# Kernel optimization log

Measured on AMD Instinct MI355X. Metric: run time of the kernel, lower is better.

Reference implementation:

```python
import jax, jax.numpy as jnp
import numpy as np

B, L1, L2 = 128, 256, 256
EMBED, HIDDEN, OUT = 512, 1024, 3


def _mlp(x, w1, b1, w2, b2):
    # MLPLayer (dropout is identity in eval): ReLU(ReLU(x W1^T + b1) W2^T + b2)
    h = jax.nn.relu(x @ w1.T + b1)
    return jax.nn.relu(h @ w2.T + b2)


def setup_inputs() -> dict:
    key = jax.random.key(0)
    ks = jax.random.split(key, 18)
    s = 0.05
    inp = {
        'sent1': jax.random.normal(ks[0], (B, L1, EMBED), jnp.float32),
        'sent2': jax.random.normal(ks[1], (B, L2, EMBED), jnp.float32),
        # attend MLP f: embed -> hidden -> hidden
        'f_w1': jax.random.normal(ks[2], (HIDDEN, EMBED), jnp.float32) * s,
        'f_b1': jnp.zeros((HIDDEN,), jnp.float32),
        'f_w2': jax.random.normal(ks[3], (HIDDEN, HIDDEN), jnp.float32) * s,
        'f_b2': jnp.zeros((HIDDEN,), jnp.float32),
        # compare MLP g: 2*embed -> hidden -> hidden
        'g_w1': jax.random.normal(ks[4], (HIDDEN, 2 * EMBED), jnp.float32) * s,
        'g_b1': jnp.zeros((HIDDEN,), jnp.float32),
        'g_w2': jax.random.normal(ks[5], (HIDDEN, HIDDEN), jnp.float32) * s,
        'g_b2': jnp.zeros((HIDDEN,), jnp.float32),
        # aggregate MLP h: 2*hidden -> hidden -> hidden
        'h_w1': jax.random.normal(ks[6], (HIDDEN, 2 * HIDDEN), jnp.float32) * s,
        'h_b1': jnp.zeros((HIDDEN,), jnp.float32),
        'h_w2': jax.random.normal(ks[7], (HIDDEN, HIDDEN), jnp.float32) * s,
        'h_b2': jnp.zeros((HIDDEN,), jnp.float32),
        # final linear: hidden -> out
        'fin_w': jax.random.normal(ks[8], (OUT, HIDDEN), jnp.float32) * s,
        'fin_b': jnp.zeros((OUT,), jnp.float32),
    }
    return inp


def reference(sent1, sent2, f_w1, f_b1, f_w2, f_b2, g_w1, g_b1, g_w2, g_b2,
              h_w1, h_b1, h_w2, h_b2, fin_w, fin_b):
    # ---- Attend ----
    f1 = _mlp(sent1, f_w1, f_b1, f_w2, f_b2)            # [B, L1, H]
    f2 = _mlp(sent2, f_w1, f_b1, f_w2, f_b2)            # [B, L2, H]
    e1 = jnp.einsum('bih,bjh->bij', f1, f2)             # [B, L1, L2], no scaling
    w1a = jax.nn.softmax(e1, axis=-1)                    # softmax over L2
    w2a = jax.nn.softmax(jnp.swapaxes(e1, 1, 2), axis=-1)  # [B, L2, L1], softmax over L1
    att1 = jnp.einsum('bij,bje->bie', w1a, sent2)       # [B, L1, E]
    att2 = jnp.einsum('bji,bie->bje', w2a, sent1)       # [B, L2, E]
    # ---- Compare ----
    cmp1 = _mlp(jnp.concatenate([att1, sent1], axis=2), g_w1, g_b1, g_w2, g_b2)  # [B, L1, H]
    cmp2 = _mlp(jnp.concatenate([att2, sent2], axis=2), g_w1, g_b1, g_w2, g_b2)  # [B, L2, H]
    # ---- Aggregate ----
    s1 = jnp.sum(cmp1, axis=1)                          # [B, H]
    s2 = jnp.sum(cmp2, axis=1)                          # [B, H]
    h = _mlp(jnp.concatenate([s1, s2], axis=1), h_w1, h_b1, h_w2, h_b2)
    return h @ fin_w.T + fin_b                          # [B, OUT]
```

## Files before the change

### kernel.cpp

```cpp
#include <hip/hip_runtime.h>
#include <hip/hip_bf16.h>


using f32x4 = __attribute__((ext_vector_type(4))) float;
using s16x8 = __attribute__((ext_vector_type(8))) short;

__device__ __forceinline__ void gload_lds16(const short* g, short* l) {
  __builtin_amdgcn_global_load_lds(
      (const __attribute__((address_space(1))) unsigned int*)g,
      (__attribute__((address_space(3))) unsigned int*)l, 16, 0, 0);
}

template <bool RELU, bool OUT_BF16, bool HAS_BIAS, bool SUML, bool CONCAT>
__global__ __launch_bounds__(256, 4) void gemm_nt(
    const short* __restrict__ A, const short* __restrict__ B,
    const float* __restrict__ bias, void* __restrict__ Cv, int K, int lda,
    int ldb, int ldc, long sA, long sB, long sC, const float* __restrict__ cs1,
    const float* __restrict__ cs2, int cBh) {
  __shared__ __align__(16) short As[128 * 64];
  __shared__ __align__(16) short Bs[128 * 64];
  const int t = threadIdx.x;
  const int lane = t & 63;
  const int wave = t >> 6;

  unsigned flat = (blockIdx.z * gridDim.y + blockIdx.y) * gridDim.x + blockIdx.x;
  const unsigned total = gridDim.x * gridDim.y * gridDim.z;
  unsigned bx = blockIdx.x, by = blockIdx.y, bz = blockIdx.z;
  if ((total & 7u) == 0) {
    unsigned nf = (flat & 7u) * (total >> 3) + (flat >> 3);
    bx = nf % gridDim.x;
    unsigned rest = nf / gridDim.x;
    by = rest % gridDim.y;
    bz = rest / gridDim.y;
  }
  const int m0 = by * 128;
  const int n0 = bx * 128;
  const long zb = bz;

  const int srow = t >> 3;
  const int schunk = ((t & 7) ^ (srow & 7)) * 8;
  const short* ag = A + zb * sA + (long)(m0 + srow) * lda + schunk;
  const short* bg = B + zb * sB + (long)(n0 + srow) * ldb + schunk;
  const long a32 = (long)32 * lda, b32 = (long)32 * ldb;
  short* AsW = As + wave * 512;
  short* BsW = Bs + wave * 512;

  const int fr = lane & 15;
  const int kq = lane >> 4;
  int aoff[4], boff[4];
#pragma unroll
  for (int i = 0; i < 4; ++i) {
    const int ra = (wave >> 1) * 64 + i * 16 + fr;
    const int rb = (wave & 1) * 64 + i * 16 + fr;
    aoff[i] = ra * 64 + ((kq ^ (ra & 7)) * 8);
    boff[i] = rb * 64 + ((kq ^ (rb & 7)) * 8);
  }

  f32x4 acc[4][4] = {};

  for (int it = K >> 6; it > 0; --it) {
    gload_lds16(ag, AsW);
    gload_lds16(ag + a32, AsW + 2048);
    gload_lds16(ag + 2 * a32, AsW + 4096);
    gload_lds16(ag + 3 * a32, AsW + 6144);
    gload_lds16(bg, BsW);
    gload_lds16(bg + b32, BsW + 2048);
    gload_lds16(bg + 2 * b32, BsW + 4096);
    gload_lds16(bg + 3 * b32, BsW + 6144);
    ag += 64;
    bg += 64;
    __syncthreads();
#pragma unroll
    for (int kk = 0; kk < 2; ++kk) {
      const int x = kk * 32;
      s16x8 af[4], bfv[4];
#pragma unroll
      for (int i = 0; i < 4; ++i) af[i] = *(const s16x8*)(As + (aoff[i] ^ x));
#pragma unroll
      for (int j = 0; j < 4; ++j) bfv[j] = *(const s16x8*)(Bs + (boff[j] ^ x));
#pragma unroll
      for (int i = 0; i < 4; ++i)
#pragma unroll
        for (int j = 0; j < 4; ++j)
          acc[i][j] = __builtin_amdgcn_mfma_f32_16x16x32_bf16(
              af[i], bfv[j], acc[i][j], 0, 0, 0);
    }
    __syncthreads();
  }

  const int ccol = lane & 15;
  const int crow = (lane >> 4) * 4;

  if constexpr (SUML) {
    __shared__ float ssum[128];
    if (t < 128) ssum[t] = 0.f;
    __syncthreads();
#pragma unroll
    for (int j = 0; j < 4; ++j) {
      const int lcol = (wave & 1) * 64 + j * 16 + ccol;
      float bj = HAS_BIAS ? bias[n0 + lcol] : 0.f;
      float part = 0.f;
#pragma unroll
      for (int i = 0; i < 4; ++i)
#pragma unroll
        for (int r = 0; r < 4; ++r) {
          float x = acc[i][j][r] + bj;
          if (RELU) x = fmaxf(x, 0.f);
          part += x;
        }
      atomicAdd(&ssum[lcol], part);
    }
    __syncthreads();
    if (t < 128) {
      const int split = (int)sC;
      int rb2 = m0 >> 8;
      const int side = rb2 >= split;
      rb2 -= side * split;
      atomicAdd((float*)Cv + (long)rb2 * ldc + side * (ldc >> 1) + n0 + t,
                ssum[t]);
    }
  } else {
#pragma unroll
    for (int j = 0; j < 4; ++j) {
      const int col = n0 + (wave & 1) * 64 + j * 16 + ccol;
      float bj = 0.f;
      if (HAS_BIAS) bj = bias[col];
#pragma unroll
      for (int i = 0; i < 4; ++i) {
        const int row0 = m0 + (wave >> 1) * 64 + i * 16 + crow;
#pragma unroll
        for (int r = 0; r < 4; ++r) {
          float x = acc[i][j][r] + bj;
          if (RELU) x = fmaxf(x, 0.f);
          const long idx = (long)(row0 + r) * ldc + col + zb * sC;
          if (OUT_BF16)
            ((__hip_bfloat16*)Cv)[idx] = __float2bfloat16(x);
          else
            ((float*)Cv)[idx] = x;
        }
      }
    }
    if constexpr (CONCAT) {
      const int side = (int)(zb >= (long)cBh);
      const int bb = (int)zb - side * cBh;
      const float* csrc = side ? cs2 : cs1;
      const long crowbase = (long)bb * 256;
      __hip_bfloat16* Cb = (__hip_bfloat16*)Cv + zb * sC + 512 + n0;
#pragma unroll
      for (int k = 0; k < 16; ++k) {
        const int idx = k * 256 + t;
        const int r = idx >> 5;
        const int q = idx & 31;
        const float4 v =
            *(const float4*)(csrc + (crowbase + m0 + r) * 512 + n0 + q * 4);
        union {
          ushort4 u;
          __hip_bfloat16 h[4];
        } pk;
        pk.h[0] = __float2bfloat16(v.x);
        pk.h[1] = __float2bfloat16(v.y);
        pk.h[2] = __float2bfloat16(v.z);
        pk.h[3] = __float2bfloat16(v.w);
        *(ushort4*)(Cb + (long)(m0 + r) * ldc + q * 4) = pk.u;
      }
    }
  }
}

struct CastArgs {
  const float* src[6];
  __hip_bfloat16* dst[6];
  long n[6];
};
__global__ void cast_many(CastArgs a) {
  const int w = blockIdx.y;
  long i = ((long)blockIdx.x * blockDim.x + threadIdx.x) * 4;
  if (i >= a.n[w]) return;
  float4 v = *(const float4*)(a.src[w] + i);
  __hip_bfloat16* o = a.dst[w] + i;
  o[0] = __float2bfloat16(v.x);
  o[1] = __float2bfloat16(v.y);
  o[2] = __float2bfloat16(v.z);
  o[3] = __float2bfloat16(v.w);
}

__global__ void cast_bf16(const float* __restrict__ in,
                          __hip_bfloat16* __restrict__ out, long n) {
  long i = ((long)blockIdx.x * blockDim.x + threadIdx.x) * 4;
  if (i >= n) return;
  float4 v = *(const float4*)(in + i);
  out[i + 0] = __float2bfloat16(v.x);
  out[i + 1] = __float2bfloat16(v.y);
  out[i + 2] = __float2bfloat16(v.z);
  out[i + 3] = __float2bfloat16(v.w);
}

__global__ void prep_sent(const float* __restrict__ s1,
                          const float* __restrict__ s2,
                          __hip_bfloat16* __restrict__ S12b,
                          __hip_bfloat16* __restrict__ STbase, int Bh) {
  __shared__ float tile[32][33];
  const int z = blockIdx.z;
  const int e0 = blockIdx.x * 32;
  const int l0 = blockIdx.y * 32;
  const int side = z >= Bh;
  const int b = z - side * Bh;
  const float* ib = (side ? s2 : s1) + (long)b * 131072;
  __hip_bfloat16* on = S12b + (long)z * 131072;
  __hip_bfloat16* ot = STbase + (long)(side ? b : (Bh + b)) * 131072;
  const int tx = threadIdx.x, ty = threadIdx.y;
#pragma unroll
  for (int k = 0; k < 4; ++k) {
    const int l = l0 + ty + 8 * k;
    const float v = ib[(long)l * 512 + e0 + tx];
    on[(long)l * 512 + e0 + tx] = __float2bfloat16(v);
    tile[ty + 8 * k][tx] = v;
  }
  __syncthreads();
#pragma unroll
  for (int k = 0; k < 4; ++k)
    ot[(long)(e0 + ty + 8 * k) * 256 + l0 + tx] =
        __float2bfloat16(tile[tx][ty + 8 * k]);
}

__global__ void softmax_rows(const float* __restrict__ E,
                             __hip_bfloat16* __restrict__ W) {
  const long row = blockIdx.x;
  const int t = threadIdx.x;
  const float x = E[row * 256 + t];
  float m = x;
  for (int o = 32; o > 0; o >>= 1) m = fmaxf(m, __shfl_xor(m, o));
  __shared__ float red[4];
  if ((t & 63) == 0) red[t >> 6] = m;
  __syncthreads();
  m = fmaxf(fmaxf(red[0], red[1]), fmaxf(red[2], red[3]));
  const float pr = __expf(x - m);
  float s = pr;
  for (int o = 32; o > 0; o >>= 1) s += __shfl_xor(s, o);
  __shared__ float red2[4];
  if ((t & 63) == 0) red2[t >> 6] = s;
  __syncthreads();
  s = red2[0] + red2[1] + red2[2] + red2[3];
  W[row * 256 + t] = __float2bfloat16(pr / s);
}

__global__ __launch_bounds__(256) void softmax_cols_f(
    const float* __restrict__ E, __hip_bfloat16* __restrict__ W) {
  __shared__ float tile[256][65];
  __shared__ float mred[4][64], sred[4][64];
  const int b = blockIdx.y;
  const int j0 = blockIdx.x * 64;
  const int t = threadIdx.x;
  const int jl = t & 63, s = t >> 6;
  const float* Eb = E + (long)b * 65536 + j0;
#pragma unroll
  for (int k = 0; k < 64; ++k) {
    const int i = k * 4 + s;
    tile[i][jl] = Eb[(long)i * 256 + jl];
  }
  __syncthreads();
  float m = -3.4e38f;
#pragma unroll 8
  for (int r = 0; r < 64; ++r) m = fmaxf(m, tile[s * 64 + r][jl]);
  mred[s][jl] = m;
  __syncthreads();
  m = fmaxf(fmaxf(mred[0][jl], mred[1][jl]), fmaxf(mred[2][jl], mred[3][jl]));
  float sum = 0.f;
#pragma unroll 8
  for (int r = 0; r < 64; ++r) sum += __expf(tile[s * 64 + r][jl] - m);
  sred[s][jl] = sum;
  __syncthreads();
  const int jw = t >> 2;
  const int ib = t & 3;
  const float mj = fmaxf(fmaxf(mred[0][jw], mred[1][jw]),
                         fmaxf(mred[2][jw], mred[3][jw]));
  const float isj =
      1.0f / (sred[0][jw] + sred[1][jw] + sred[2][jw] + sred[3][jw]);
  __hip_bfloat16* Wb = W + (long)b * 65536 + (long)(j0 + jw) * 256 + ib * 64;
#pragma unroll 8
  for (int r = 0; r < 64; ++r)
    Wb[r] = __float2bfloat16(__expf(tile[ib * 64 + r][jw] - mj) * isj);
}

__global__ void final_lin(const __hip_bfloat16* __restrict__ h2,
                          const float* __restrict__ w,
                          const float* __restrict__ bs,
                          float* __restrict__ out) {
  const int b = blockIdx.x;
  const int t = threadIdx.x;
  float p0 = 0.f, p1 = 0.f, p2 = 0.f;
  for (int k = t; k < 1024; k += 256) {
    const float x = __bfloat162float(h2[(long)b * 1024 + k]);
    p0 += x * w[k];
    p1 += x * w[1024 + k];
    p2 += x * w[2048 + k];
  }
  for (int o = 32; o > 0; o >>= 1) {
    p0 += __shfl_xor(p0, o);
    p1 += __shfl_xor(p1, o);
    p2 += __shfl_xor(p2, o);
  }
  __shared__ float r[4][3];
  if ((t & 63) == 0) {
    r[t >> 6][0] = p0;
    r[t >> 6][1] = p1;
    r[t >> 6][2] = p2;
  }
  __syncthreads();
  if (t < 3)
    out[b * 3 + t] = r[0][t] + r[1][t] + r[2][t] + r[3][t] + bs[t];
}

extern "C" void kernel_launch(void* const* d_in, const int* in_sizes, int n_in,
                              void* d_out, int out_size, void* d_ws,
                              size_t ws_size, hipStream_t stream) {
  const float* sent1 = (const float*)d_in[0];
  const float* sent2 = (const float*)d_in[1];
  const float* f_w1 = (const float*)d_in[2];
  const float* f_b1 = (const float*)d_in[3];
  const float* f_w2 = (const float*)d_in[4];
  const float* f_b2 = (const float*)d_in[5];
  const float* g_w1 = (const float*)d_in[6];
  const float* g_b1 = (const float*)d_in[7];
  const float* g_w2 = (const float*)d_in[8];
  const float* g_b2 = (const float*)d_in[9];
  const float* h_w1 = (const float*)d_in[10];
  const float* h_b1 = (const float*)d_in[11];
  const float* h_w2 = (const float*)d_in[12];
  const float* h_b2 = (const float*)d_in[13];
  const float* fin_w = (const float*)d_in[14];
  const float* fin_b = (const float*)d_in[15];

  char* p = (char*)d_ws;
  auto take = [&](size_t n) {
    char* r = p;
    p += (n + 255) & ~(size_t)255;
    return r;
  };
  const int Bh = (ws_size >= (size_t)220 * 1024 * 1024) ? 64 : 32;
  const int chunks = 128 / Bh;
  const long R = (long)Bh * 256;

  short* Wf1 = (short*)take(1024L * 512 * 2);
  short* Wf2 = (short*)take(1024L * 1024 * 2);
  short* Wg1 = (short*)take(1024L * 1024 * 2);
  short* Wg2 = (short*)take(1024L * 1024 * 2);
  short* Wh1 = (short*)take(1024L * 2048 * 2);
  short* Wh2 = (short*)take(1024L * 1024 * 2);
  float* SUMF = (float*)take(128L * 2048 * 4);
  short* scat = (short*)take(128L * 2048 * 2);
  short* hh = (short*)take(128L * 1024 * 2);
  short* hf = (short*)take(128L * 1024 * 2);
  char* Areg = take(2 * R * 1024 * 2);
  char* Breg = take(2 * R * 1024 * 2);
  char* Creg = take(2 * R * 512 * 2);
  char* Dreg = take(2 * R * 512 * 2);
  (void)in_sizes; (void)n_in; (void)out_size;

  short* FHID = (short*)Areg;
  short* GHID = (short*)Areg;
  short* F12 = (short*)Breg;
  short* CC12 = (short*)Breg;
  short* S12b = (short*)Creg;
  float* E1 = (float*)Creg;
  short* W1A = (short*)(Creg + (long)Bh * 262144);
  short* W2A = W1A + (long)Bh * 65536;
  short* ST = (short*)Dreg;

  hipMemsetAsync(SUMF, 0, 128L * 2048 * 4, stream);

  CastArgs ca;
  ca.src[0] = f_w1; ca.dst[0] = (__hip_bfloat16*)Wf1; ca.n[0] = 524288;
  ca.src[1] = f_w2; ca.dst[1] = (__hip_bfloat16*)Wf2; ca.n[1] = 1048576;
  ca.src[2] = g_w1; ca.dst[2] = (__hip_bfloat16*)Wg1; ca.n[2] = 1048576;
  ca.src[3] = g_w2; ca.dst[3] = (__hip_bfloat16*)Wg2; ca.n[3] = 1048576;
  ca.src[4] = h_w1; ca.dst[4] = (__hip_bfloat16*)Wh1; ca.n[4] = 2097152;
  ca.src[5] = h_w2; ca.dst[5] = (__hip_bfloat16*)Wh2; ca.n[5] = 1048576;
  cast_many<<<dim3(2048, 6), 256, 0, stream>>>(ca);

  for (int c = 0; c < chunks; ++c) {
    const float* s1 = sent1 + (long)c * R * 512;
    const float* s2 = sent2 + (long)c * R * 512;
    float* SUMF_c = SUMF + (long)c * Bh * 2048;
    const int MT = (int)(2 * R / 128);

    prep_sent<<<dim3(16, 8, 2 * Bh), dim3(32, 8), 0, stream>>>(
        s1, s2, (__hip_bfloat16*)S12b, (__hip_bfloat16*)ST, Bh);

    gemm_nt<true, true, true, false, false><<<dim3(8, MT, 1), 256, 0, stream>>>(
        S12b, Wf1, f_b1, FHID, 512, 512, 512, 1024, 0, 0, 0, nullptr, nullptr, 0);
    gemm_nt<true, true, true, false, false><<<dim3(8, MT, 1), 256, 0, stream>>>(
        FHID, Wf2, f_b2, F12, 1024, 1024, 1024, 1024, 0, 0, 0, nullptr, nullptr, 0);

    gemm_nt<false, false, false, false, false><<<dim3(2, 2, Bh), 256, 0, stream>>>(
        F12, F12 + R * 1024, nullptr, E1, 1024, 1024, 1024, 256, 256L * 1024,
        256L * 1024, 65536, nullptr, nullptr, 0);

    softmax_rows<<<Bh * 256, 256, 0, stream>>>(E1, (__hip_bfloat16*)W1A);
    softmax_cols_f<<<dim3(4, Bh), 256, 0, stream>>>(E1, (__hip_bfloat16*)W2A);

    gemm_nt<false, true, false, false, true><<<dim3(4, 2, 2 * Bh), 256, 0, stream>>>(
        W1A, ST, nullptr, CC12, 256, 256, 256, 1024, 65536, 131072, 262144,
        s1, s2, Bh);

    gemm_nt<true, true, true, false, false><<<dim3(8, MT, 1), 256, 0, stream>>>(
        CC12, Wg1, g_b1, GHID, 1024, 1024, 1024, 1024, 0, 0, 0, nullptr, nullptr, 0);
    gemm_nt<true, false, true, true, false><<<dim3(8, MT, 1), 256, 0, stream>>>(
        GHID, Wg2, g_b2, SUMF_c, 1024, 1024, 1024, 2048, 0, 0, Bh, nullptr, nullptr, 0);
  }

  cast_bf16<<<256, 256, 0, stream>>>(SUMF, (__hip_bfloat16*)scat, 262144);
  gemm_nt<true, true, true, false, false><<<dim3(8, 1, 1), 256, 0, stream>>>(
      scat, Wh1, h_b1, hh, 2048, 2048, 2048, 1024, 0, 0, 0, nullptr, nullptr, 0);
  gemm_nt<true, true, true, false, false><<<dim3(8, 1, 1), 256, 0, stream>>>(
      hh, Wh2, h_b2, hf, 1024, 1024, 1024, 1024, 0, 0, 0, nullptr, nullptr, 0);
  final_lin<<<128, 256, 0, stream>>>((__hip_bfloat16*)hf, fin_w, fin_b,
                                     (float*)d_out);
}
```

Measured before the change: 901.5 us.

## Add 256x256-tile 8-wave pipelined GEMM for the four big MLP layers

Adds a new GEMM kernel with 256x256 output tiles, 512 threads and a four-stage LDS pipeline built on direct global-to-LDS loads. Reads from LDS and MFMA work are interleaved through explicit barriers, waitcnt instructions and priority hints, with XOR swizzling to avoid bank conflicts. The kernel replaces the 128-tile kernel for the f and g MLP GEMMs, and its sum variant first reduces over rows in LDS before issuing global atomics. Larger tiles raise arithmetic intensity and reuse, at the cost of fewer blocks, lower occupancy and more register pressure.

```diff
diff --git a/kernel.cpp b/kernel.cpp
--- a/kernel.cpp
+++ b/kernel.cpp
@@ -9,6 +9,223 @@
   __builtin_amdgcn_global_load_lds(
       (const __attribute__((address_space(1))) unsigned int*)g,
       (__attribute__((address_space(3))) unsigned int*)l, 16, 0, 0);
+}
+
+template <bool SUML>
+__global__ __launch_bounds__(512, 2) void gemm256(
+    const short* __restrict__ A, const short* __restrict__ B,
+    const float* __restrict__ bias, void* __restrict__ Cv, int K, int lda,
+    int ldb, int ldc, int split) {
+  __shared__ __align__(16) short As[2 * 2 * 8192];
+  __shared__ __align__(16) short Bs[2 * 2 * 8192];
+
+  const int t = threadIdx.x;
+  const int lane = t & 63;
+  const int w = t >> 6;
+  const int wm = w >> 2;
+  const int wn = w & 3;
+
+  unsigned bx = blockIdx.x, by = blockIdx.y;
+  {
+    unsigned flat = by * gridDim.x + bx;
+    unsigned total = gridDim.x * gridDim.y;
+    if ((total & 7u) == 0) {
+      unsigned nf = (flat & 7u) * (total >> 3) + (flat >> 3);
+      bx = nf % gridDim.x;
+      by = nf / gridDim.x;
+    }
+  }
+  const int m0 = by * 256;
+  const int n0 = bx * 256;
+
+  const short* gA[2];
+  const short* gB[2];
+  short* lA[2];
+  short* lB[2];
+#pragma unroll
+  for (int q = 0; q < 2; ++q) {
+    const int r = (w * 2 + q) * 16 + (lane >> 2);
+    const int cg = (lane & 3) ^ ((r >> 1) & 3);
+    gA[q] = A + (long)(m0 + r) * lda + cg * 8;
+    gB[q] = B + (long)(n0 + r) * ldb + cg * 8;
+    lA[q] = As + (w * 2 + q) * 512;
+    lB[q] = Bs + (w * 2 + q) * 512;
+  }
+
+  const int c4 = lane >> 4;
+  const int rA0 = wm * 128 + (lane & 15);
+  const int rB0 = wn * 64 + (lane & 15);
+  const int aoff0 = rA0 * 32 + ((c4 ^ ((rA0 >> 1) & 3)) * 8);
+  const int boff0 = rB0 * 32 + ((c4 ^ ((rB0 >> 1) & 3)) * 8);
+
+  f32x4 acc[8][4] = {};
+  s16x8 af[8], bf[2];
+
+  const int nIter = K >> 7;
+
+  auto stgA = [&](int koff, int roff) {
+#pragma unroll
+    for (int q = 0; q < 2; ++q) gload_lds16(gA[q] + koff, lA[q] + roff);
+  };
+  auto stgB = [&](int koff, int roff) {
+#pragma unroll
+    for (int q = 0; q < 2; ++q) gload_lds16(gB[q] + koff, lB[q] + roff);
+  };
+  auto rdA = [&](int reg) {
+#pragma unroll
+    for (int m = 0; m < 8; ++m)
+      af[m] = *(const s16x8*)(As + reg + aoff0 + m * 512);
+  };
+  auto rdB = [&](int reg, int np) {
+#pragma unroll
+    for (int n = 0; n < 2; ++n)
+      bf[n] = *(const s16x8*)(Bs + reg + boff0 + (np * 2 + n) * 512);
+  };
+  auto mf16 = [&](int np) {
+    __builtin_amdgcn_s_setprio(1);
+#pragma unroll
+    for (int m = 0; m < 8; ++m)
+#pragma unroll
+      for (int n = 0; n < 2; ++n)
+        acc[m][np * 2 + n] = __builtin_amdgcn_mfma_f32_16x16x32_bf16(
+            af[m], bf[n], acc[m][np * 2 + n], 0, 0, 0);
+    __builtin_amdgcn_s_setprio(0);
+  };
+
+  stgA(0, 0);
+  stgB(0, 0);
+  stgA(32, 8192);
+  stgB(32, 8192);
+  stgA(64, 16384);
+  stgB(64, 16384);
+  asm volatile("s_waitcnt vmcnt(4)" ::: "memory");
+  __builtin_amdgcn_sched_barrier(0);
+  __builtin_amdgcn_s_barrier();
+
+  for (int i = 0; i < nIter; ++i) {
+    const int kb = i * 128;
+    const bool more = (i + 1 < nIter);
+
+    rdA(0);
+    rdB(0, 0);
+    stgA(kb + 96, 24576);
+    __builtin_amdgcn_s_barrier();
+    asm volatile("s_waitcnt lgkmcnt(0)" ::: "memory");
+    __builtin_amdgcn_sched_barrier(0);
+    mf16(0);
+    __builtin_amdgcn_s_barrier();
+
+    rdB(0, 1);
+    stgB(kb + 96, 24576);
+    __builtin_amdgcn_s_barrier();
+    asm volatile("s_waitcnt lgkmcnt(0)" ::: "memory");
+    __builtin_amdgcn_sched_barrier(0);
+    mf16(1);
+    __builtin_amdgcn_s_barrier();
+
+    rdA(8192);
+    rdB(8192, 0);
+    if (more) stgA(kb + 128, 0);
+    __builtin_amdgcn_s_barrier();
+    asm volatile("s_waitcnt lgkmcnt(0)" ::: "memory");
+    __builtin_amdgcn_sched_barrier(0);
+    mf16(0);
+    __builtin_amdgcn_s_barrier();
+
+    rdB(8192, 1);
+    if (more) stgB(kb + 128, 0);
+    __builtin_amdgcn_s_barrier();
+    asm volatile("s_waitcnt lgkmcnt(0)" ::: "memory");
+    __builtin_amdgcn_sched_barrier(0);
+    mf16(1);
+    if (more) {
+      asm volatile("s_waitcnt vmcnt(4)" ::: "memory");
+    } else {
+      asm volatile("s_waitcnt vmcnt(0)" ::: "memory");
+    }
+    __builtin_amdgcn_sched_barrier(0);
+    __builtin_amdgcn_s_barrier();
+
+    rdA(16384);
+    rdB(16384, 0);
+    if (more) stgA(kb + 160, 8192);
+    __builtin_amdgcn_s_barrier();
+    asm volatile("s_waitcnt lgkmcnt(0)" ::: "memory");
+    __builtin_amdgcn_sched_barrier(0);
+    mf16(0);
+    __builtin_amdgcn_s_barrier();
+
+    rdB(16384, 1);
+    if (more) stgB(kb + 160, 8192);
+    __builtin_amdgcn_s_barrier();
+    asm volatile("s_waitcnt lgkmcnt(0)" ::: "memory");
+    __builtin_amdgcn_sched_barrier(0);
+    mf16(1);
+    __builtin_amdgcn_s_barrier();
+
+    rdA(24576);
+    rdB(24576, 0);
+    if (more) stgA(kb + 192, 16384);
+    __builtin_amdgcn_s_barrier();
+    asm volatile("s_waitcnt lgkmcnt(0)" ::: "memory");
+    __builtin_amdgcn_sched_barrier(0);
+    mf16(0);
+    __builtin_amdgcn_s_barrier();
+
+    rdB(24576, 1);
+    if (more) stgB(kb + 192, 16384);
+    __builtin_amdgcn_s_barrier();
+    asm volatile("s_waitcnt lgkmcnt(0)" ::: "memory");
+    __builtin_amdgcn_sched_barrier(0);
+    mf16(1);
+    asm volatile("s_waitcnt vmcnt(4)" ::: "memory");
+    __builtin_amdgcn_sched_barrier(0);
+    __builtin_amdgcn_s_barrier();
+  }
+
+  const int ccol = lane & 15;
+  const int crow = (lane >> 4) * 4;
+  if constexpr (!SUML) {
+#pragma unroll
+    for (int j = 0; j < 4; ++j) {
+      const int col = n0 + wn * 64 + j * 16 + ccol;
+      const float bj = bias[col];
+#pragma unroll
+      for (int m = 0; m < 8; ++m) {
+        const int row0 = m0 + wm * 128 + m * 16 + crow;
+#pragma unroll
+        for (int r = 0; r < 4; ++r) {
+          float x = fmaxf(acc[m][j][r] + bj, 0.f);
+          ((__hip_bfloat16*)Cv)[(long)(row0 + r) * ldc + col] =
+              __float2bfloat16(x);
+        }
+      }
+    }
+  } else {
+    __shared__ float ssum[256];
+    __syncthreads();
+    if (t < 256) ssum[t] = 0.f;
+    __syncthreads();
+#pragma unroll
+    for (int j = 0; j < 4; ++j) {
+      const int lcol = wn * 64 + j * 16 + ccol;
+      const float bj = bias[n0 + lcol];
+      float part = 0.f;
+#pragma unroll
+      for (int m = 0; m < 8; ++m)
+#pragma unroll
+        for (int r = 0; r < 4; ++r) part += fmaxf(acc[m][j][r] + bj, 0.f);
+      atomicAdd(&ssum[lcol], part);
+    }
+    __syncthreads();
+    if (t < 256) {
+      int rb2 = m0 >> 8;
+      const int side = rb2 >= split;
+      rb2 -= side * split;
+      atomicAdd((float*)Cv + (long)rb2 * ldc + side * (ldc >> 1) + n0 + t,
+                ssum[t]);
+    }
+  }
 }
 
 template <bool RELU, bool OUT_BF16, bool HAS_BIAS, bool SUML, bool CONCAT>
@@ -382,15 +599,15 @@
     const float* s1 = sent1 + (long)c * R * 512;
     const float* s2 = sent2 + (long)c * R * 512;
     float* SUMF_c = SUMF + (long)c * Bh * 2048;
-    const int MT = (int)(2 * R / 128);
+    const int MT2 = (int)(2 * R / 256);
 
     prep_sent<<<dim3(16, 8, 2 * Bh), dim3(32, 8), 0, stream>>>(
         s1, s2, (__hip_bfloat16*)S12b, (__hip_bfloat16*)ST, Bh);
 
-    gemm_nt<true, true, true, false, false><<<dim3(8, MT, 1), 256, 0, stream>>>(
-        S12b, Wf1, f_b1, FHID, 512, 512, 512, 1024, 0, 0, 0, nullptr, nullptr, 0);
-    gemm_nt<true, true, true, false, false><<<dim3(8, MT, 1), 256, 0, stream>>>(
-        FHID, Wf2, f_b2, F12, 1024, 1024, 1024, 1024, 0, 0, 0, nullptr, nullptr, 0);
+    gemm256<false><<<dim3(4, MT2), 512, 0, stream>>>(
+        S12b, Wf1, f_b1, FHID, 512, 512, 512, 1024, 0);
+    gemm256<false><<<dim3(4, MT2), 512, 0, stream>>>(
+        FHID, Wf2, f_b2, F12, 1024, 1024, 1024, 1024, 0);
 
     gemm_nt<false, false, false, false, false><<<dim3(2, 2, Bh), 256, 0, stream>>>(
         F12, F12 + R * 1024, nullptr, E1, 1024, 1024, 1024, 256, 256L * 1024,
@@ -403,10 +620,10 @@
         W1A, ST, nullptr, CC12, 256, 256, 256, 1024, 65536, 131072, 262144,
         s1, s2, Bh);
 
-    gemm_nt<true, true, true, false, false><<<dim3(8, MT, 1), 256, 0, stream>>>(
-        CC12, Wg1, g_b1, GHID, 1024, 1024, 1024, 1024, 0, 0, 0, nullptr, nullptr, 0);
-    gemm_nt<true, false, true, true, false><<<dim3(8, MT, 1), 256, 0, stream>>>(
-        GHID, Wg2, g_b2, SUMF_c, 1024, 1024, 1024, 2048, 0, 0, Bh, nullptr, nullptr, 0);
+    gemm256<false><<<dim3(4, MT2), 512, 0, stream>>>(
+        CC12, Wg1, g_b1, GHID, 1024, 1024, 1024, 1024, 0);
+    gemm256<true><<<dim3(4, MT2), 512, 0, stream>>>(
+        GHID, Wg2, g_b2, SUMF_c, 1024, 1024, 1024, 2048, Bh);
   }
 
   cast_bf16<<<256, 256, 0, stream>>>(SUMF, (__hip_bfloat16*)scat, 262144);
```

Result: slower. 1.061 ms (+17.6%).

## Fuse attention score GEMM with row softmax in one kernel

Applied to the files above, without the earlier changes.

Replaces the batched E1 GEMM plus separate row-softmax kernel with a single kernel that computes a 64x256 tile of scores per block and applies the row softmax in registers before writing both fp32 scores and bf16 weights. This removes a kernel launch and the re-read of E1 for the row softmax. The new kernel uses 64-row tiles, a large B tile in LDS and 16 accumulators per thread, and has no double buffering, so MFMA utilization may drop compared with the generic GEMM.

```diff
diff --git a/kernel.cpp b/kernel.cpp
--- a/kernel.cpp
+++ b/kernel.cpp
@@ -167,6 +167,96 @@
   }
 }
 
+__global__ __launch_bounds__(256, 4) void e1_rowsm(
+    const short* __restrict__ A, const short* __restrict__ B,
+    float* __restrict__ E, __hip_bfloat16* __restrict__ W) {
+  __shared__ __align__(16) short As[64 * 64];
+  __shared__ __align__(16) short Bs[256 * 64];
+  const int t = threadIdx.x;
+  const int lane = t & 63;
+  const int w = t >> 6;
+  const int m0 = blockIdx.x * 64;
+  const long z = blockIdx.y;
+
+  const int srow = t >> 3;
+  const int schunk = ((t & 7) ^ (srow & 7)) * 8;
+  const short* ag = A + z * 262144 + (long)(m0 + srow) * 1024 + schunk;
+  const short* bg = B + z * 262144 + (long)srow * 1024 + schunk;
+  short* AsW = As + w * 512;
+  short* BsW = Bs + w * 512;
+
+  const int fr = lane & 15;
+  const int kq = lane >> 4;
+  const int ra = w * 16 + fr;
+  const int aoff = ra * 64 + ((kq ^ (ra & 7)) * 8);
+  int boff[16];
+#pragma unroll
+  for (int j = 0; j < 16; ++j) {
+    const int rb = j * 16 + fr;
+    boff[j] = rb * 64 + ((kq ^ (rb & 7)) * 8);
+  }
+
+  f32x4 acc[16] = {};
+
+  for (int it = 0; it < 16; ++it) {
+    gload_lds16(ag, AsW);
+    gload_lds16(ag + 32768, AsW + 2048);
+#pragma unroll
+    for (int q = 0; q < 8; ++q)
+      gload_lds16(bg + (long)q * 32768, BsW + q * 2048);
+    ag += 64;
+    bg += 64;
+    __syncthreads();
+#pragma unroll
+    for (int kk = 0; kk < 2; ++kk) {
+      const int x = kk * 32;
+      const s16x8 af = *(const s16x8*)(As + (aoff ^ x));
+#pragma unroll
+      for (int j = 0; j < 16; ++j) {
+        const s16x8 bf = *(const s16x8*)(Bs + (boff[j] ^ x));
+        acc[j] = __builtin_amdgcn_mfma_f32_16x16x32_bf16(af, bf, acc[j], 0, 0, 0);
+      }
+    }
+    __syncthreads();
+  }
+
+  const int crow = kq * 4;
+  float mx[4] = {-3.4e38f, -3.4e38f, -3.4e38f, -3.4e38f};
+#pragma unroll
+  for (int j = 0; j < 16; ++j)
+#pragma unroll
+    for (int r = 0; r < 4; ++r) mx[r] = fmaxf(mx[r], acc[j][r]);
+#pragma unroll
+  for (int o = 1; o < 16; o <<= 1)
+#pragma unroll
+    for (int r = 0; r < 4; ++r) mx[r] = fmaxf(mx[r], __shfl_xor(mx[r], o));
+  float sm[4] = {0.f, 0.f, 0.f, 0.f};
+#pragma unroll
+  for (int j = 0; j < 16; ++j)
+#pragma unroll
+    for (int r = 0; r < 4; ++r) sm[r] += __expf(acc[j][r] - mx[r]);
+#pragma unroll
+  for (int o = 1; o < 16; o <<= 1)
+#pragma unroll
+    for (int r = 0; r < 4; ++r) sm[r] += __shfl_xor(sm[r], o);
+  float is[4];
+#pragma unroll
+  for (int r = 0; r < 4; ++r) is[r] = 1.0f / sm[r];
+
+  float* Eb = E + z * 65536;
+  __hip_bfloat16* Wb = W + z * 65536;
+#pragma unroll
+  for (int j = 0; j < 16; ++j) {
+    const int col = j * 16 + fr;
+#pragma unroll
+    for (int r = 0; r < 4; ++r) {
+      const long idx = (long)(m0 + w * 16 + crow + r) * 256 + col;
+      Eb[idx] = acc[j][r];
+      Wb[idx] = __float2bfloat16(__expf(acc[j][r] - mx[r]) * is[r]);
+    }
+  }
+}
+
 struct CastArgs {
   const float* src[6];
   __hip_bfloat16* dst[6];
@@ -221,27 +311,6 @@
   for (int k = 0; k < 4; ++k)
     ot[(long)(e0 + ty + 8 * k) * 256 + l0 + tx] =
         __float2bfloat16(tile[tx][ty + 8 * k]);
-}
-
-__global__ void softmax_rows(const float* __restrict__ E,
-                             __hip_bfloat16* __restrict__ W) {
-  const long row = blockIdx.x;
-  const int t = threadIdx.x;
-  const float x = E[row * 256 + t];
-  float m = x;
-  for (int o = 32; o > 0; o >>= 1) m = fmaxf(m, __shfl_xor(m, o));
-  __shared__ float red[4];
-  if ((t & 63) == 0) red[t >> 6] = m;
-  __syncthreads();
-  m = fmaxf(fmaxf(red[0], red[1]), fmaxf(red[2], red[3]));
-  const float pr = __expf(x - m);
-  float s = pr;
-  for (int o = 32; o > 0; o >>= 1) s += __shfl_xor(s, o);
-  __shared__ float red2[4];
-  if ((t & 63) == 0) red2[t >> 6] = s;
-  __syncthreads();
-  s = red2[0] + red2[1] + red2[2] + red2[3];
-  W[row * 256 + t] = __float2bfloat16(pr / s);
 }
 
 __global__ __launch_bounds__(256) void softmax_cols_f(
@@ -392,11 +461,9 @@
     gemm_nt<true, true, true, false, false><<<dim3(8, MT, 1), 256, 0, stream>>>(
         FHID, Wf2, f_b2, F12, 1024, 1024, 1024, 1024, 0, 0, 0, nullptr, nullptr, 0);
 
-    gemm_nt<false, false, false, false, false><<<dim3(2, 2, Bh), 256, 0, stream>>>(
-        F12, F12 + R * 1024, nullptr, E1, 1024, 1024, 1024, 256, 256L * 1024,
-        256L * 1024, 65536, nullptr, nullptr, 0);
-
-    softmax_rows<<<Bh * 256, 256, 0, stream>>>(E1, (__hip_bfloat16*)W1A);
+    e1_rowsm<<<dim3(4, Bh), 256, 0, stream>>>(
+        F12, F12 + R * 1024, E1, (__hip_bfloat16*)W1A);
+
     softmax_cols_f<<<dim3(4, Bh), 256, 0, stream>>>(E1, (__hip_bfloat16*)W2A);
 
     gemm_nt<false, true, false, false, true><<<dim3(4, 2, 2 * Bh), 256, 0, stream>>>(
```

After: 936.5 us. 3.9% more time.
